# Kernel optimization log

Hardware: AMD Instinct MI355X
Metric: run time of the kernel (lower is better)

The kernel has to match this reference:

```python
import jax, jax.numpy as jnp
import numpy as np

B, C, H, W = 4, 512, 64, 64
INTER = 64  # C // channel_stride


def setup_inputs() -> dict:
    key = jax.random.key(0)
    ks = jax.random.split(key, 5)
    s = 0.02  # small init scale for numerical stability of softmax logits
    return {
        "inputs": jax.random.normal(ks[0], (B, C, H, W), dtype=jnp.float32),
        "Wq": jax.random.normal(ks[1], (INTER, C), dtype=jnp.float32) * s,
        "bq": jnp.zeros((INTER,), dtype=jnp.float32),
        "Wk": jax.random.normal(ks[2], (INTER, C), dtype=jnp.float32) * s,
        "bk": jnp.zeros((INTER,), dtype=jnp.float32),
        "Wv": jax.random.normal(ks[3], (C, C), dtype=jnp.float32) * s,
        "bv": jnp.zeros((C,), dtype=jnp.float32),
        "gamma": jax.random.normal(ks[4], (1,), dtype=jnp.float32),
    }


def reference(inputs, Wq, bq, Wk, bk, Wv, bv, gamma):
    b, c, h, w = inputs.shape
    n = h * w
    x = inputs.reshape(b, c, n)  # (B, C, N)
    # 1x1 convs == per-pixel linear projections
    q = jnp.einsum('dc,bcn->bnd', Wq, x) + bq            # (B, N, d)
    k = jnp.einsum('dc,bcn->bdn', Wk, x) + bk[:, None]   # (B, d, N)
    v = jnp.einsum('oc,bcn->bon', Wv, x) + bv[:, None]   # (B, O, N)
    # affinity: (B, Nq, Nk), softmax over keys (last dim), no scaling (as in source)
    affinity = jax.nn.softmax(jnp.einsum('bnd,bdm->bnm', q, k), axis=-1)
    # note: torch does bmm(value, affinity) -> out[b,o,m] = sum_j v[b,o,j] * A[b,j,m]
    out = jnp.einsum('bon,bnm->bom', v, affinity)        # (B, O, N)
    return gamma * out.reshape(b, -1, h, w) + inputs
```

## Files before the change

### kernel.cpp

```cpp
#include <hip/hip_runtime.h>
#include <stdint.h>

typedef __attribute__((ext_vector_type(8))) short short8;
typedef __attribute__((ext_vector_type(4))) float f32x4;
typedef __attribute__((ext_vector_type(8))) unsigned short u16x8;
typedef __attribute__((ext_vector_type(4))) unsigned short u16x4;
typedef __attribute__((ext_vector_type(2))) unsigned short u16x2;
typedef unsigned short u16;

#define NPIX 4096
#define CCH  512
#define DD   64


__device__ inline float b2f(u16 h){
  union { unsigned int i; float f; } u; u.i = ((unsigned int)h) << 16; return u.f;
}
__device__ inline u16 f2b(float f){
  union { float f; unsigned int i; } u; u.f = f;
  return (u16)((u.i + 0x7fffu + ((u.i >> 16) & 1u)) >> 16);
}
__device__ inline void gl2lds16(const void* g, void* l){
  __builtin_amdgcn_global_load_lds((const __attribute__((address_space(1))) unsigned int*)g,
                                   (__attribute__((address_space(3))) unsigned int*)l, 16, 0, 0);
}
__device__ inline f32x4 mfma16(short8 a, short8 b, f32x4 c){
  return __builtin_amdgcn_mfma_f32_16x16x32_bf16(a, b, c, 0, 0, 0);
}

__global__ __launch_bounds__(256) void k0_transpose(const float* __restrict__ x,
    u16* __restrict__ xT, const float* __restrict__ Wq, const float* __restrict__ Wk,
    const float* __restrict__ Wv, u16* __restrict__ Wqkb, u16* __restrict__ Wvb){
  if (blockIdx.z == 4){
    int bid = blockIdx.x * 8 + blockIdx.y;
    for (int r = 0; r < 3; ++r){
      int i = (r * 512 + bid) * 256 + threadIdx.x;
      if (i < 65536){
        int row = i >> 9, col = i & 511;
        float v = (row < 64) ? Wq[(row << 9) + col] : Wk[((row - 64) << 9) + col];
        Wqkb[(row << 9) + (col ^ ((row & 7) << 3))] = f2b(v);
      } else if (i < 327680){
        int j = i - 65536;
        int row = j >> 9, col = j & 511;
        Wvb[(row << 9) + (col ^ ((row & 7) << 3))] = f2b(Wv[j]);
      }
    }
    return;
  }
  __shared__ u16 tile[64][66];
  const int b = blockIdx.z;
  const int n0 = blockIdx.x * 64, c0 = blockIdx.y * 64;
  const float* xb = x + ((size_t)b * CCH + c0) * NPIX + n0;
  #pragma unroll
  for (int r = 0; r < 16; ++r){
    int id = r * 256 + threadIdx.x;
    int cc = id >> 6, nn = id & 63;
    tile[nn][cc] = f2b(xb[(size_t)cc * NPIX + nn]);
  }
  __syncthreads();
  u16* xTb = xT + ((size_t)b * NPIX + n0) * CCH + c0;
  #pragma unroll
  for (int r = 0; r < 8; ++r){
    int id = r * 256 + threadIdx.x;
    int nn = id >> 5, c2 = id & 31;
    int colp = (2 * c2) ^ ((nn & 7) << 3);
    *(u16x2*)(xTb + (size_t)nn * CCH + colp) = *(const u16x2*)&tile[nn][2 * c2];
  }
}

__global__ __launch_bounds__(256) void k1_qk(const u16* __restrict__ xT,
    const u16* __restrict__ Wqk, const float* __restrict__ bq,
    const float* __restrict__ bk, u16* __restrict__ Qb, u16* __restrict__ Kb){
  __shared__ __align__(16) u16 As[128*64];
  __shared__ __align__(16) u16 Bs[128*64];
  const int b  = blockIdx.z;
  const int n0 = blockIdx.x * 128;
  const u16* Ab = xT + ((size_t)b * NPIX + n0) * CCH;
  const int t = threadIdx.x, wave = t >> 6, lane = t & 63, q = lane >> 4, l16 = lane & 15;
  const int wr = (wave >> 1) * 64, wc = (wave & 1) * 64;
  const int sw = l16 & 7;
  f32x4 acc[4][4];
  #pragma unroll
  for (int i = 0; i < 4; ++i)
    #pragma unroll
    for (int j = 0; j < 4; ++j) acc[i][j] = (f32x4){0.f,0.f,0.f,0.f};

  for (int k0 = 0; k0 < CCH; k0 += 64){
    __syncthreads();
    #pragma unroll
    for (int r = 0; r < 4; ++r){
      int id = r * 256 + t;
      int row = id >> 3, ko = (id & 7) << 3;
      gl2lds16(Ab + (size_t)row * CCH + k0 + ko, &As[id * 8]);
      gl2lds16(Wqk + (size_t)row * CCH + k0 + ko, &Bs[id * 8]);
    }
    __syncthreads();
    #pragma unroll
    for (int s = 0; s < 2; ++s){
      const int ca = ((s*4 + q) ^ sw) << 3;
      short8 af[4], bfr[4];
      #pragma unroll
      for (int i = 0; i < 4; ++i){
        af[i]  = *(const short8*)&As[(wr + i*16 + l16)*64 + ca];
        bfr[i] = *(const short8*)&Bs[(wc + i*16 + l16)*64 + ca];
      }
      #pragma unroll
      for (int i = 0; i < 4; ++i)
        #pragma unroll
        for (int j = 0; j < 4; ++j)
          acc[i][j] = mfma16(af[i], bfr[j], acc[i][j]);
    }
  }
  #pragma unroll
  for (int i = 0; i < 4; ++i){
    #pragma unroll
    for (int j = 0; j < 4; ++j){
      int col = wc + j*16 + l16;
      #pragma unroll
      for (int r2 = 0; r2 < 4; ++r2){
        int n = n0 + wr + i*16 + q*4 + r2;
        int sw8 = (n & 7) << 3;
        float v = acc[i][j][r2];
        if (col < 64) Qb[((size_t)b * NPIX + n) * DD + (col ^ sw8)]        = f2b(v + bq[col]);
        else          Kb[((size_t)b * NPIX + n) * DD + ((col - 64) ^ sw8)] = f2b(v + bk[col - 64]);
      }
    }
  }
}

__global__ __launch_bounds__(256) void k2_v(const u16* __restrict__ xT,
    const u16* __restrict__ Wvb, const float* __restrict__ bv, u16* __restrict__ Vb){
  __shared__ __align__(16) u16 As[128*64];
  __shared__ __align__(16) u16 Bs[128*64];
  const int b  = blockIdx.z;
  const int n0 = blockIdx.x * 128;
  const int o0 = blockIdx.y * 128;
  const u16* Ab = Wvb + (size_t)o0 * CCH;
  const u16* Bb = xT + ((size_t)b * NPIX + n0) * CCH;
  const int t = threadIdx.x, wave = t >> 6, lane = t & 63, q = lane >> 4, l16 = lane & 15;
  const int wr = (wave >> 1) * 64, wc = (wave & 1) * 64;
  const int sw = l16 & 7;
  f32x4 acc[4][4];
  #pragma unroll
  for (int i = 0; i < 4; ++i)
    #pragma unroll
    for (int j = 0; j < 4; ++j) acc[i][j] = (f32x4){0.f,0.f,0.f,0.f};

  for (int k0 = 0; k0 < CCH; k0 += 64){
    __syncthreads();
    #pragma unroll
    for (int r = 0; r < 4; ++r){
      int id = r * 256 + t;
      int row = id >> 3, ko = (id & 7) << 3;
      gl2lds16(Ab + (size_t)row * CCH + k0 + ko, &As[id * 8]);
      gl2lds16(Bb + (size_t)row * CCH + k0 + ko, &Bs[id * 8]);
    }
    __syncthreads();
    #pragma unroll
    for (int s = 0; s < 2; ++s){
      const int ca = ((s*4 + q) ^ sw) << 3;
      short8 af[4], bfr[4];
      #pragma unroll
      for (int i = 0; i < 4; ++i){
        af[i]  = *(const short8*)&As[(wr + i*16 + l16)*64 + ca];
        bfr[i] = *(const short8*)&Bs[(wc + i*16 + l16)*64 + ca];
      }
      #pragma unroll
      for (int i = 0; i < 4; ++i)
        #pragma unroll
        for (int j = 0; j < 4; ++j)
          acc[i][j] = mfma16(af[i], bfr[j], acc[i][j]);
    }
  }
  #pragma unroll
  for (int i = 0; i < 4; ++i){
    #pragma unroll
    for (int j = 0; j < 4; ++j){
      int n = n0 + wc + j*16 + l16;
      #pragma unroll
      for (int r2 = 0; r2 < 4; ++r2){
        int o = o0 + wr + i*16 + q*4 + r2;
        int np = n ^ ((o & 7) << 3);
        Vb[((size_t)b * CCH + o) * NPIX + np] = f2b(acc[i][j][r2] + bv[o]);
      }
    }
  }
}

__global__ __launch_bounds__(256) void k3_logits(const u16* __restrict__ Qb,
    const u16* __restrict__ Kb, u16* __restrict__ E, float* __restrict__ Z, int b0){
  __shared__ __align__(16) u16 smem[128*136];
  u16* As = smem;
  u16* Bs = smem + 128*64;
  const int bloc = blockIdx.z, b = b0 + bloc;
  const int n0 = blockIdx.x * 128;
  const int m0 = blockIdx.y * 128;
  const u16* Ab = Kb + ((size_t)b * NPIX + m0) * DD;
  const u16* Bb = Qb + ((size_t)b * NPIX + n0) * DD;
  const int t = threadIdx.x, wave = t >> 6, lane = t & 63, q = lane >> 4, l16 = lane & 15;
  const int wr = (wave >> 1) * 64, wc = (wave & 1) * 64;
  const int sw = l16 & 7;
  f32x4 acc[4][4];
  #pragma unroll
  for (int i = 0; i < 4; ++i)
    #pragma unroll
    for (int j = 0; j < 4; ++j) acc[i][j] = (f32x4){0.f,0.f,0.f,0.f};

  #pragma unroll
  for (int r = 0; r < 4; ++r){
    int id = r * 256 + t;
    int row = id >> 3, ko = (id & 7) << 3;
    gl2lds16(Ab + row * DD + ko, &As[id * 8]);
    gl2lds16(Bb + row * DD + ko, &Bs[id * 8]);
  }
  __syncthreads();
  #pragma unroll
  for (int s = 0; s < 2; ++s){
    const int ca = ((s*4 + q) ^ sw) << 3;
    short8 af[4], bfr[4];
    #pragma unroll
    for (int i = 0; i < 4; ++i){
      af[i]  = *(const short8*)&As[(wr + i*16 + l16)*64 + ca];
      bfr[i] = *(const short8*)&Bs[(wc + i*16 + l16)*64 + ca];
    }
    #pragma unroll
    for (int i = 0; i < 4; ++i)
      #pragma unroll
      for (int j = 0; j < 4; ++j)
        acc[i][j] = mfma16(af[i], bfr[j], acc[i][j]);
  }
  __syncthreads();
  u16* tile = smem;
  float colsum[4] = {0.f, 0.f, 0.f, 0.f};
  #pragma unroll
  for (int i = 0; i < 4; ++i){
    #pragma unroll
    for (int j = 0; j < 4; ++j){
      #pragma unroll
      for (int r2 = 0; r2 < 4; ++r2){
        int mrow = wr + i*16 + q*4 + r2;
        int ncol = wc + j*16 + l16;
        float l = fminf(fmaxf(acc[i][j][r2], -60.f), 30.f);
        float e = __expf(l);
        tile[mrow * 136 + ncol] = f2b(e);
        colsum[j] += e;
      }
    }
  }
  #pragma unroll
  for (int j = 0; j < 4; ++j){
    float v = colsum[j];
    v += __shfl_xor(v, 16, 64);
    v += __shfl_xor(v, 32, 64);
    if (q == 0) atomicAdd(&Z[(size_t)b * NPIX + n0 + wc + j*16 + l16], v);
  }
  __syncthreads();
  u16* Eb = E + (size_t)bloc * NPIX * NPIX;
  #pragma unroll
  for (int r = 0; r < 8; ++r){
    int id = r * 256 + t;
    int row = id >> 4, chunk = id & 15;
    int g = chunk >> 3, c3 = chunk & 7;
    int colp = g * 64 + ((c3 ^ (row & 7)) << 3);
    *(u16x8*)(Eb + (size_t)(m0 + row) * NPIX + n0 + colp) =
        *(const u16x8*)&tile[row * 136 + chunk * 8];
  }
}

__global__ __launch_bounds__(256) void k3b_scale(u16* __restrict__ Vb,
    const float* __restrict__ Z, const float* __restrict__ gm, int b0){
  size_t i4  = ((size_t)blockIdx.x * 256 + threadIdx.x) * 4;
  size_t off = ((size_t)b0 << 21) + i4;
  int b = (int)(off >> 21);
  int o = (int)((off >> 12) & 511);
  int np = (int)(off & (NPIX - 1));
  int nl = np ^ ((o & 7) << 3);
  float g = gm[0];
  u16x4 vv = *(const u16x4*)(Vb + off);
  f32x4 zz = *(const f32x4*)(Z + ((size_t)b << 12) + nl);
  u16x4 r;
  #pragma unroll
  for (int k = 0; k < 4; ++k) r[k] = f2b(g * b2f(vv[k]) / fmaxf(zz[k], 1e-20f));
  *(u16x4*)(Vb + off) = r;
}

__global__ __launch_bounds__(512, 2) void k4_out(const u16* __restrict__ Vs,
    const u16* __restrict__ E, const float* __restrict__ xin,
    float* __restrict__ outp, int b0){
  __shared__ __align__(16) u16 As[3][128*64];
  __shared__ __align__(16) u16 Bs[3][256*64];
  const int bloc = blockIdx.z, b = b0 + bloc;
  const int m0 = blockIdx.x * 256;
  const int o0 = blockIdx.y * 128;
  const u16* Ab = Vs + ((size_t)b * CCH + o0) * NPIX;
  const u16* Bb = E + (size_t)bloc * NPIX * NPIX + (size_t)m0 * NPIX;
  const int t = threadIdx.x, wave = t >> 6, lane = t & 63, q = lane >> 4, l16 = lane & 15;
  const int ar = (wave >> 2) * 64;
  const int br = (wave & 3) * 64;
  const int sw = l16 & 7;

  auto stageA = [&](int kt, int bi){
    const int k0 = kt << 6;
    #pragma unroll
    for (int r = 0; r < 2; ++r){
      int id = r * 512 + t;
      gl2lds16(Ab + (size_t)(id >> 3) * NPIX + (k0 + ((id & 7) << 3)), &As[bi][id * 8]);
    }
  };
  auto stageBh = [&](int kt, int bi, int half){
    const int k0 = kt << 6;
    #pragma unroll
    for (int r = 0; r < 2; ++r){
      int id = (half * 2 + r) * 512 + t;
      gl2lds16(Bb + (size_t)(id >> 3) * NPIX + (k0 + ((id & 7) << 3)), &Bs[bi][id * 8]);
    }
  };

  f32x4 acc[4][4];
  #pragma unroll
  for (int i = 0; i < 4; ++i)
    #pragma unroll
    for (int j = 0; j < 4; ++j) acc[i][j] = (f32x4){0.f,0.f,0.f,0.f};

  stageA(0, 0); stageBh(0, 0, 0); stageBh(0, 0, 1);
  stageA(1, 1); stageBh(1, 1, 0); stageBh(1, 1, 1);
  asm volatile("s_waitcnt vmcnt(6)" ::: "memory");
  __builtin_amdgcn_sched_barrier(0);
  __builtin_amdgcn_s_barrier();

  int bi = 0;
  for (int kt = 0; kt < NPIX / 64; ++kt){
    const int bi2 = (bi >= 1) ? bi - 1 : bi + 2;
    const bool pf = (kt + 2) < NPIX / 64;
    short8 af[4], bfr[4];
    {
      const int ca = (q ^ sw) << 3;
      #pragma unroll
      for (int i = 0; i < 4; ++i) af[i]  = *(const short8*)&As[bi][(ar + i*16 + l16)*64 + ca];
      #pragma unroll
      for (int j = 0; j < 4; ++j) bfr[j] = *(const short8*)&Bs[bi][(br + j*16 + l16)*64 + ca];
      if (pf){ stageA(kt + 2, bi2); stageBh(kt + 2, bi2, 0); }
      __builtin_amdgcn_s_barrier();
      asm volatile("s_waitcnt lgkmcnt(0)" ::: "memory");
      __builtin_amdgcn_sched_barrier(0);
      __builtin_amdgcn_s_setprio(1);
      #pragma unroll
      for (int i = 0; i < 4; ++i)
        #pragma unroll
        for (int j = 0; j < 4; ++j)
          acc[i][j] = mfma16(af[i], bfr[j], acc[i][j]);
      __builtin_amdgcn_s_setprio(0);
      __builtin_amdgcn_s_barrier();
    }
    {
      const int ca = ((4 + q) ^ sw) << 3;
      #pragma unroll
      for (int i = 0; i < 4; ++i) af[i]  = *(const short8*)&As[bi][(ar + i*16 + l16)*64 + ca];
      #pragma unroll
      for (int j = 0; j < 4; ++j) bfr[j] = *(const short8*)&Bs[bi][(br + j*16 + l16)*64 + ca];
      if (pf) stageBh(kt + 2, bi2, 1);
      __builtin_amdgcn_s_barrier();
      asm volatile("s_waitcnt lgkmcnt(0)" ::: "memory");
      __builtin_amdgcn_sched_barrier(0);
      __builtin_amdgcn_s_setprio(1);
      #pragma unroll
      for (int i = 0; i < 4; ++i)
        #pragma unroll
        for (int j = 0; j < 4; ++j)
          acc[i][j] = mfma16(af[i], bfr[j], acc[i][j]);
      __builtin_amdgcn_s_setprio(0);
      if (kt < NPIX / 64 - 2){ asm volatile("s_waitcnt vmcnt(6)" ::: "memory"); }
      else                   { asm volatile("s_waitcnt vmcnt(0)" ::: "memory"); }
      __builtin_amdgcn_sched_barrier(0);
      __builtin_amdgcn_s_barrier();
    }
    bi = (bi == 2) ? 0 : bi + 1;
  }

  const float* xb = xin + (size_t)b * CCH * NPIX;
  float* ob = outp + (size_t)b * CCH * NPIX;
  #pragma unroll
  for (int i = 0; i < 4; ++i){
    #pragma unroll
    for (int j = 0; j < 4; ++j){
      int m = m0 + br + j*16 + l16;
      #pragma unroll
      for (int r2 = 0; r2 < 4; ++r2){
        int o = o0 + ar + i*16 + q*4 + r2;
        size_t idx = (size_t)o * NPIX + m;
        ob[idx] = acc[i][j][r2] + xb[idx];
      }
    }
  }
}

extern "C" void kernel_launch(void* const* d_in, const int* in_sizes, int n_in,
                              void* d_out, int out_size, void* d_ws, size_t ws_size,
                              hipStream_t stream){
  (void)in_sizes; (void)n_in; (void)out_size;
  const float* x  = (const float*)d_in[0];
  const float* Wq = (const float*)d_in[1];
  const float* bq = (const float*)d_in[2];
  const float* Wk = (const float*)d_in[3];
  const float* bk = (const float*)d_in[4];
  const float* Wv = (const float*)d_in[5];
  const float* bv = (const float*)d_in[6];
  const float* gm = (const float*)d_in[7];
  float* outp = (float*)d_out;

  char* ws = (char*)d_ws;
  u16*  Qb   = (u16*)(ws + 0);
  u16*  Kb   = (u16*)(ws + 2097152);
  u16*  Vb   = (u16*)(ws + 4194304);
  float* Z   = (float*)(ws + 20971520);
  u16*  Wqkb = (u16*)(ws + 21037056);
  u16*  Wvb  = (u16*)(ws + 21168128);
  u16*  xT   = (u16*)(ws + 21692416);
  u16*  E    = (u16*)(ws + 21692416);

  const size_t ebytes = (size_t)NPIX * NPIX * 2;
  const size_t base   = 21692416;
  if (ws_size < base + ebytes){
    return;
  }
  int NB = 1;
  if (ws_size >= base + 4 * ebytes) NB = 4;
  else if (ws_size >= base + 2 * ebytes) NB = 2;

  hipMemsetAsync(Z, 0, (size_t)4 * NPIX * sizeof(float), stream);
  k0_transpose<<<dim3(64, 8, 5), 256, 0, stream>>>(x, xT, Wq, Wk, Wv, Wqkb, Wvb);
  k1_qk<<<dim3(32, 1, 4), 256, 0, stream>>>(xT, Wqkb, bq, bk, Qb, Kb);
  k2_v<<<dim3(32, 4, 4), 256, 0, stream>>>(xT, Wvb, bv, Vb);
  for (int b0 = 0; b0 < 4; b0 += NB){
    int nb = NB; if (b0 + nb > 4) nb = 4 - b0;
    k3_logits<<<dim3(32, 32, nb), 256, 0, stream>>>(Qb, Kb, E, Z, b0);
    k3b_scale<<<dim3(nb * 2048), 256, 0, stream>>>(Vb, Z, gm, b0);
    k4_out<<<dim3(16, 4, nb), 512, 0, stream>>>(Vb, E, x, outp, b0);
  }
}
```

Measured before the change: 243.2 us.

## Split K across wave groups in k4_out with LDS reduction of partial sums

Waves are now split into two groups that each cover all 128 output rows. Each group handles half of the 64-wide K chunk instead of covering half the rows, so each tile iteration issues one barrier-separated phase instead of two. The two groups' partial accumulators are reduced through LDS at the end before the residual add. This doubles accumulator registers per wave and adds an epilogue reduction, in exchange for fewer barriers and LDS read phases in the main loop.

New measurement: 232.3 us (median of 2 runs). -4.5%, faster.

```diff
diff --git a/kernel.cpp b/kernel.cpp
--- a/kernel.cpp
+++ b/kernel.cpp
@@ -287,108 +287,103 @@
 __global__ __launch_bounds__(512, 2) void k4_out(const u16* __restrict__ Vs,
     const u16* __restrict__ E, const float* __restrict__ xin,
     float* __restrict__ outp, int b0){
-  __shared__ __align__(16) u16 As[3][128*64];
-  __shared__ __align__(16) u16 Bs[3][256*64];
+  __shared__ __align__(16) u16 smem[3*128*64 + 3*256*64];
+  u16* As = smem;
+  u16* Bs = smem + 3*128*64;
   const int bloc = blockIdx.z, b = b0 + bloc;
   const int m0 = blockIdx.x * 256;
   const int o0 = blockIdx.y * 128;
   const u16* Ab = Vs + ((size_t)b * CCH + o0) * NPIX;
   const u16* Bb = E + (size_t)bloc * NPIX * NPIX + (size_t)m0 * NPIX;
   const int t = threadIdx.x, wave = t >> 6, lane = t & 63, q = lane >> 4, l16 = lane & 15;
-  const int ar = (wave >> 2) * 64;
-  const int br = (wave & 3) * 64;
+  const int grp = wave >> 2;
+  const int br  = (wave & 3) * 64;
   const int sw = l16 & 7;
+  const int ca = ((grp * 4 + q) ^ sw) << 3;
 
   auto stageA = [&](int kt, int bi){
     const int k0 = kt << 6;
+    u16* dst = As + bi * (128*64);
     #pragma unroll
     for (int r = 0; r < 2; ++r){
       int id = r * 512 + t;
-      gl2lds16(Ab + (size_t)(id >> 3) * NPIX + (k0 + ((id & 7) << 3)), &As[bi][id * 8]);
+      gl2lds16(Ab + (size_t)(id >> 3) * NPIX + (k0 + ((id & 7) << 3)), dst + id * 8);
     }
   };
-  auto stageBh = [&](int kt, int bi, int half){
+  auto stageB = [&](int kt, int bi){
     const int k0 = kt << 6;
-    #pragma unroll
-    for (int r = 0; r < 2; ++r){
-      int id = (half * 2 + r) * 512 + t;
-      gl2lds16(Bb + (size_t)(id >> 3) * NPIX + (k0 + ((id & 7) << 3)), &Bs[bi][id * 8]);
+    u16* dst = Bs + bi * (256*64);
+    #pragma unroll
+    for (int r = 0; r < 4; ++r){
+      int id = r * 512 + t;
+      gl2lds16(Bb + (size_t)(id >> 3) * NPIX + (k0 + ((id & 7) << 3)), dst + id * 8);
     }
   };
 
-  f32x4 acc[4][4];
-  #pragma unroll
-  for (int i = 0; i < 4; ++i)
+  f32x4 acc[8][4];
+  #pragma unroll
+  for (int i = 0; i < 8; ++i)
     #pragma unroll
     for (int j = 0; j < 4; ++j) acc[i][j] = (f32x4){0.f,0.f,0.f,0.f};
 
-  stageA(0, 0); stageBh(0, 0, 0); stageBh(0, 0, 1);
-  stageA(1, 1); stageBh(1, 1, 0); stageBh(1, 1, 1);
+  stageA(0, 0); stageB(0, 0);
+  stageA(1, 1); stageB(1, 1);
   asm volatile("s_waitcnt vmcnt(6)" ::: "memory");
   __builtin_amdgcn_sched_barrier(0);
   __builtin_amdgcn_s_barrier();
 
   int bi = 0;
   for (int kt = 0; kt < NPIX / 64; ++kt){
-    const int bi2 = (bi >= 1) ? bi - 1 : bi + 2;
+    const int bi2 = (bi >= 1) ? bi - 1 : 2;
     const bool pf = (kt + 2) < NPIX / 64;
-    short8 af[4], bfr[4];
-    {
-      const int ca = (q ^ sw) << 3;
-      #pragma unroll
-      for (int i = 0; i < 4; ++i) af[i]  = *(const short8*)&As[bi][(ar + i*16 + l16)*64 + ca];
-      #pragma unroll
-      for (int j = 0; j < 4; ++j) bfr[j] = *(const short8*)&Bs[bi][(br + j*16 + l16)*64 + ca];
-      if (pf){ stageA(kt + 2, bi2); stageBh(kt + 2, bi2, 0); }
-      __builtin_amdgcn_s_barrier();
-      asm volatile("s_waitcnt lgkmcnt(0)" ::: "memory");
-      __builtin_amdgcn_sched_barrier(0);
-      __builtin_amdgcn_s_setprio(1);
-      #pragma unroll
-      for (int i = 0; i < 4; ++i)
+    const u16* Ap = As + bi * (128*64);
+    const u16* Bp = Bs + bi * (256*64);
+    short8 af[8], bfr[4];
+    #pragma unroll
+    for (int i = 0; i < 8; ++i) af[i]  = *(const short8*)&Ap[(i*16 + l16)*64 + ca];
+    #pragma unroll
+    for (int j = 0; j < 4; ++j) bfr[j] = *(const short8*)&Bp[(br + j*16 + l16)*64 + ca];
+    if (pf){ stageA(kt + 2, bi2); stageB(kt + 2, bi2); }
+    asm volatile("s_waitcnt lgkmcnt(0)" ::: "memory");
+    __builtin_amdgcn_sched_barrier(0);
+    __builtin_amdgcn_s_setprio(1);
+    #pragma unroll
+    for (int i = 0; i < 8; ++i)
+      #pragma unroll
+      for (int j = 0; j < 4; ++j)
+        acc[i][j] = mfma16(af[i], bfr[j], acc[i][j]);
+    __builtin_amdgcn_s_setprio(0);
+    if (pf){ asm volatile("s_waitcnt vmcnt(6)" ::: "memory"); }
+    else   { asm volatile("s_waitcnt vmcnt(0)" ::: "memory"); }
+    __builtin_amdgcn_sched_barrier(0);
+    __builtin_amdgcn_s_barrier();
+    bi = (bi == 2) ? 0 : bi + 1;
+  }
+
+  float* red = (float*)smem;
+  if (grp == 1){
+    #pragma unroll
+    for (int i = 0; i < 8; ++i)
+      #pragma unroll
+      for (int j = 0; j < 4; ++j)
+        *(f32x4*)&red[(size_t)(br + j*16 + l16) * 132 + i*16 + q*4] = acc[i][j];
+  }
+  __syncthreads();
+  if (grp == 0){
+    const float* xb = xin + (size_t)b * CCH * NPIX;
+    float* ob = outp + (size_t)b * CCH * NPIX;
+    #pragma unroll
+    for (int i = 0; i < 8; ++i){
+      #pragma unroll
+      for (int j = 0; j < 4; ++j){
+        f32x4 p = *(const f32x4*)&red[(size_t)(br + j*16 + l16) * 132 + i*16 + q*4];
+        int m = m0 + br + j*16 + l16;
         #pragma unroll
-        for (int j = 0; j < 4; ++j)
-          acc[i][j] = mfma16(af[i], bfr[j], acc[i][j]);
-      __builtin_amdgcn_s_setprio(0);
-      __builtin_amdgcn_s_barrier();
-    }
-    {
-      const int ca = ((4 + q) ^ sw) << 3;
-      #pragma unroll
-      for (int i = 0; i < 4; ++i) af[i]  = *(const short8*)&As[bi][(ar + i*16 + l16)*64 + ca];
-      #pragma unroll
-      for (int j = 0; j < 4; ++j) bfr[j] = *(const short8*)&Bs[bi][(br + j*16 + l16)*64 + ca];
-      if (pf) stageBh(kt + 2, bi2, 1);
-      __builtin_amdgcn_s_barrier();
-      asm volatile("s_waitcnt lgkmcnt(0)" ::: "memory");
-      __builtin_amdgcn_sched_barrier(0);
-      __builtin_amdgcn_s_setprio(1);
-      #pragma unroll
-      for (int i = 0; i < 4; ++i)
-        #pragma unroll
-        for (int j = 0; j < 4; ++j)
-          acc[i][j] = mfma16(af[i], bfr[j], acc[i][j]);
-      __builtin_amdgcn_s_setprio(0);
-      if (kt < NPIX / 64 - 2){ asm volatile("s_waitcnt vmcnt(6)" ::: "memory"); }
-      else                   { asm volatile("s_waitcnt vmcnt(0)" ::: "memory"); }
-      __builtin_amdgcn_sched_barrier(0);
-      __builtin_amdgcn_s_barrier();
-    }
-    bi = (bi == 2) ? 0 : bi + 1;
-  }
-
-  const float* xb = xin + (size_t)b * CCH * NPIX;
-  float* ob = outp + (size_t)b * CCH * NPIX;
-  #pragma unroll
-  for (int i = 0; i < 4; ++i){
-    #pragma unroll
-    for (int j = 0; j < 4; ++j){
-      int m = m0 + br + j*16 + l16;
-      #pragma unroll
-      for (int r2 = 0; r2 < 4; ++r2){
-        int o = o0 + ar + i*16 + q*4 + r2;
-        size_t idx = (size_t)o * NPIX + m;
-        ob[idx] = acc[i][j][r2] + xb[idx];
+        for (int r2 = 0; r2 < 4; ++r2){
+          int o = o0 + i*16 + q*4 + r2;
+          size_t idx = (size_t)o * NPIX + m;
+          ob[idx] = acc[i][j][r2] + p[r2] + xb[idx];
+        }
       }
     }
   }
```
